# Kernel tuning notes

Measured on AMD Instinct MI355X. Metric: run time of the kernel, lower is better.

## Reference

```python
import jax, jax.numpy as jnp
import numpy as np
import math

WS = 7          # window_size
TOPK = 4        # routed regions
NUM_HEADS = 8   # only used for the scale factor (heads never split in forward)


def _dwconv(v_img, kernel, bias):
    # v_img: (N, ws, ws, C); kernel: (3, 3, 1, C) depthwise (groups=C), padding=1
    out = jax.lax.conv_general_dilated(
        v_img, kernel, window_strides=(1, 1), padding='SAME',
        dimension_numbers=('NHWC', 'HWIO', 'NHWC'),
        feature_group_count=v_img.shape[-1])
    return out + bias


def setup_inputs() -> dict:
    key = jax.random.key(0)
    ks = jax.random.split(key, 12)
    B, H, W, C = 8, 56, 56, 256
    std = 0.02
    return {
        'x': jax.random.normal(ks[0], (B, H, W, C), jnp.float32),
        'w_qkv': jax.random.normal(ks[1], (C, 3 * C), jnp.float32) * std,
        'b_qkv': jnp.zeros((3 * C,), jnp.float32),
        'w_g1': jax.random.normal(ks[2], (C, C // 4), jnp.float32) * std,
        'b_g1': jnp.zeros((C // 4,), jnp.float32),
        'w_g2': jax.random.normal(ks[3], (C // 4, 2), jnp.float32) * std,
        'b_g2': jnp.zeros((2,), jnp.float32),
        'dw_kernel': jax.random.normal(ks[4], (3, 3, 1, C), jnp.float32) * std,
        'dw_bias': jnp.zeros((C,), jnp.float32),
        'w_proj': jax.random.normal(ks[5], (C, C), jnp.float32) * std,
        'b_proj': jnp.zeros((C,), jnp.float32),
    }


def reference(x, w_qkv, b_qkv, w_g1, b_g1, w_g2, b_g2, dw_kernel, dw_bias, w_proj, b_proj):
    B, H, W, C = x.shape
    ws = WS
    nH, nW = H // ws, W // ws      # input chosen divisible by ws (pad path is no-op)
    S, ntok = nH * nW, ws * ws
    t = min(TOPK, S)
    scale = (C // NUM_HEADS) ** (-0.5)

    # window partition: (B, S, ws*ws, C)
    xw = x.reshape(B, nH, ws, nW, ws, C).transpose(0, 1, 3, 2, 4, 5).reshape(B, S, ntok, C)
    x_region = xw.mean(axis=2)                                  # (B, S, C)

    # region-level qkv and routing scores
    qkv_r = (x_region @ w_qkv + b_qkv).reshape(B, S, 3, C)
    q_r, k_r = qkv_r[:, :, 0], qkv_r[:, :, 1]
    A_r = jnp.einsum('bsc,bzc->bsz', q_r, k_r) * scale          # (B, S, S)
    _, topk_idx = jax.lax.top_k(A_r, t)                         # (B, S, t)

    # per-region Gaussian (diagonal covariance) weights over regions
    gp = jax.nn.relu(q_r @ w_g1 + b_g1) @ w_g2 + b_g2           # (B, S, 2)
    sigma = jax.nn.softplus(gp) + 0.5
    s_side = int(round(math.sqrt(S)))
    coords = jnp.arange(s_side, dtype=x.dtype)
    gy, gx = jnp.meshgrid(coords, coords, indexing='ij')
    mu = jnp.stack([gx.ravel(), gy.ravel()], axis=-1)           # (S, 2) as (x, y)
    d = mu[None, :, :] - mu[:, None, :]                         # (S, S, 2): mu_j - mu_i
    z = (d[..., 0][None] / sigma[..., 0][:, :, None]) ** 2 \
        + (d[..., 1][None] / sigma[..., 1][:, :, None]) ** 2    # (B, S, S)
    gauss = jnp.exp(-0.5 * z)
    gauss = gauss / (gauss.sum(-1, keepdims=True) + 1e-6)
    gwt = jnp.take_along_axis(gauss, topk_idx, axis=2)          # (B, S, t)

    # token-level qkv within windows
    qkv = (xw @ w_qkv + b_qkv).reshape(B, S, ntok, 3, C)
    q, k, v = qkv[..., 0, :], qkv[..., 1, :], qkv[..., 2, :]    # (B, S, ntok, C)

    # gather routed windows and reweight by Gaussian
    gather = jax.vmap(lambda a, i: a[i])                        # over batch
    k_g = (gather(k, topk_idx) * gwt[..., None, None]).reshape(B, S, t * ntok, C)
    v_g = (gather(v, topk_idx) * gwt[..., None, None]).reshape(B, S, t * ntok, C)

    attn = jax.nn.softmax(jnp.einsum('bswc,bskc->bswk', q, k_g) * scale, axis=-1)
    out = jnp.einsum('bswk,bskc->bswc', attn, v_g)              # (B, S, ntok, C)

    # depthwise-conv branch on v
    vdw = _dwconv(v.reshape(B * S, ws, ws, C), dw_kernel, dw_bias).reshape(B, S, ntok, C)
    out = out + vdw

    # window merge + output projection
    out = out.reshape(B, nH, nW, ws, ws, C).transpose(0, 1, 3, 2, 4, 5).reshape(B, H, W, C)
    return out @ w_proj + b_proj
```

## Files before the change

kernel.cpp:

```cpp
#include <hip/hip_runtime.h>
#include <math.h>

#define SCALE 0.17677669529663687f

typedef short short8 __attribute__((ext_vector_type(8)));
typedef float f32x4 __attribute__((ext_vector_type(4)));

__device__ __forceinline__ int token_row_addr(int m) {
    int b = m / 3136;
    int rem = m - b * 3136;
    int s = rem / 49;
    int tok = rem - s * 49;
    int h = (s >> 3) * 7 + tok / 7;
    int w = (s & 7) * 7 + (tok % 7);
    return (b * 56 + h) * 56 + w;
}

__device__ __forceinline__ void split2(float x, unsigned short& h, unsigned short& l) {
    unsigned int u = __float_as_uint(x);
    h = (unsigned short)(u >> 16);
    float hf = __uint_as_float(u & 0xFFFF0000u);
    l = (unsigned short)(__float_as_uint(x - hf) >> 16);
}

__device__ __forceinline__ unsigned int pack2(float x) {
    unsigned short h, l;
    split2(x, h, l);
    return ((unsigned int)h << 16) | l;
}

__device__ __forceinline__ float b2f(unsigned short u) {
    return __uint_as_float(((unsigned int)u) << 16);
}

__device__ __forceinline__ float unpack_f(unsigned int u) {
    return b2f((unsigned short)(u >> 16)) + b2f((unsigned short)(u & 0xFFFFu));
}

__device__ __forceinline__ void unpack_u4(uint4 a, uint4 b, short8& h, short8& l) {
    h[0] = (short)(a.x >> 16); l[0] = (short)(a.x & 0xFFFFu);
    h[1] = (short)(a.y >> 16); l[1] = (short)(a.y & 0xFFFFu);
    h[2] = (short)(a.z >> 16); l[2] = (short)(a.z & 0xFFFFu);
    h[3] = (short)(a.w >> 16); l[3] = (short)(a.w & 0xFFFFu);
    h[4] = (short)(b.x >> 16); l[4] = (short)(b.x & 0xFFFFu);
    h[5] = (short)(b.y >> 16); l[5] = (short)(b.y & 0xFFFFu);
    h[6] = (short)(b.z >> 16); l[6] = (short)(b.z & 0xFFFFu);
    h[7] = (short)(b.w >> 16); l[7] = (short)(b.w & 0xFFFFu);
}

__device__ __forceinline__ void load_unpack8(const unsigned int* g, short8& h, short8& l) {
    uint4 a = *(const uint4*)g;
    uint4 b = *(const uint4*)(g + 4);
    unpack_u4(a, b, h, l);
}

__device__ __forceinline__ void gload16(const unsigned short* g, unsigned short* l) {
    __builtin_amdgcn_global_load_lds(
        (const __attribute__((address_space(1))) unsigned int*)g,
        (__attribute__((address_space(3))) unsigned int*)l, 16, 0, 0);
}

__global__ void k_cvt_x(const float* __restrict__ x, unsigned short* __restrict__ xhi,
                        unsigned short* __restrict__ xlo) {
    int m = blockIdx.x;
    int k = threadIdx.x;
    float v = x[(size_t)token_row_addr(m) * 256 + k];
    unsigned short h, l;
    split2(v, h, l);
    xhi[(size_t)m * 256 + k] = h;
    xlo[(size_t)m * 256 + k] = l;
}

__global__ void k_cvt_w(const float* __restrict__ w, int ncols,
                        unsigned short* __restrict__ whi, unsigned short* __restrict__ wlo) {
    int n = blockIdx.x;
    int k = threadIdx.x;
    float v = w[(size_t)k * ncols + n];
    unsigned short h, l;
    split2(v, h, l);
    whi[(size_t)n * 256 + k] = h;
    wlo[(size_t)n * 256 + k] = l;
}

__global__ void k_region_mean(const float* __restrict__ x, float* __restrict__ xr) {
    int blk = blockIdx.x;
    int b = blk >> 6, s = blk & 63;
    int c = threadIdx.x;
    int hy0 = (s >> 3) * 7, wx0 = (s & 7) * 7;
    const float* xb = x + ((size_t)b * 56 * 56) * 256 + c;
    float sum = 0.f;
#pragma unroll 1
    for (int t = 0; t < 49; ++t) {
        int h = hy0 + t / 7, w = wx0 + (t % 7);
        sum += xb[(size_t)(h * 56 + w) * 256];
    }
    xr[(size_t)blk * 256 + c] = sum * (1.0f / 49.0f);
}

__global__ void k_region_qkv(const float* __restrict__ xr, const float* __restrict__ wqkv,
                             const float* __restrict__ bqkv, float* __restrict__ qkvr) {
    __shared__ float xs[256];
    int blk = blockIdx.x;
    int t = threadIdx.x;
    xs[t] = xr[(size_t)blk * 256 + t];
    __syncthreads();
    float a0 = 0.f, a1 = 0.f, a2 = 0.f;
#pragma unroll 4
    for (int k = 0; k < 256; ++k) {
        float xv = xs[k];
        const float* wrow = wqkv + (size_t)k * 768;
        a0 += xv * wrow[t];
        a1 += xv * wrow[t + 256];
        a2 += xv * wrow[t + 512];
    }
    float* o = qkvr + (size_t)blk * 768;
    o[t]       = a0 + bqkv[t];
    o[t + 256] = a1 + bqkv[t + 256];
    o[t + 512] = a2 + bqkv[t + 512];
}

__global__ void k_gating(const float* __restrict__ qkvr, const float* __restrict__ wg1,
                         const float* __restrict__ bg1, const float* __restrict__ wg2,
                         const float* __restrict__ bg2, float* __restrict__ sig) {
    __shared__ float hs[64];
    int blk = blockIdx.x;
    int j = threadIdx.x;
    const float* qr = qkvr + (size_t)blk * 768;
    float acc = bg1[j];
#pragma unroll 4
    for (int k = 0; k < 256; ++k) acc += qr[k] * wg1[(size_t)k * 64 + j];
    hs[j] = fmaxf(acc, 0.f);
    __syncthreads();
    if (j < 2) {
        float gp = bg2[j];
#pragma unroll 1
        for (int m = 0; m < 64; ++m) gp += hs[m] * wg2[m * 2 + j];
        float sp = fmaxf(gp, 0.f) + log1pf(expf(-fabsf(gp)));
        sig[blk * 2 + j] = sp + 0.5f;
    }
}

__global__ void k_topk_gauss(const float* __restrict__ qkvr, const float* __restrict__ sig,
                             int* __restrict__ topk, float* __restrict__ gwt) {
    __shared__ float A[64];
    __shared__ float G[64];
    __shared__ int idxs[4];
    __shared__ float gsum_s;
    int blk = blockIdx.x;
    int b = blk >> 6, s = blk & 63;
    int z = threadIdx.x;
    const float* qr = qkvr + (size_t)blk * 768;
    const float* kr = qkvr + (size_t)(b * 64 + z) * 768 + 256;
    float acc = 0.f;
#pragma unroll 4
    for (int k = 0; k < 256; k += 4) {
        float4 q4 = *(const float4*)(qr + k);
        float4 k4 = *(const float4*)(kr + k);
        acc += q4.x * k4.x + q4.y * k4.y + q4.z * k4.z + q4.w * k4.w;
    }
    A[z] = acc * SCALE;
    float s0 = sig[blk * 2 + 0], s1 = sig[blk * 2 + 1];
    float dx = (float)((z & 7) - (s & 7));
    float dy = (float)((z >> 3) - (s >> 3));
    float t0 = dx / s0, t1 = dy / s1;
    float zz = t0 * t0 + t1 * t1;
    G[z] = expf(-0.5f * zz);
    __syncthreads();
    if (z == 0) {
        float gs = 0.f;
        for (int m = 0; m < 64; ++m) gs += G[m];
        gsum_s = gs + 1e-6f;
        for (int it = 0; it < 4; ++it) {
            int best = 0;
            float bv = A[0];
            for (int m = 1; m < 64; ++m) {
                if (A[m] > bv) { bv = A[m]; best = m; }
            }
            idxs[it] = best;
            A[best] = -3.0e38f;
        }
    }
    __syncthreads();
    if (z < 4) {
        int id = idxs[z];
        topk[blk * 4 + z] = id;
        gwt[blk * 4 + z] = G[id] / gsum_s;
    }
}

__global__ __launch_bounds__(256) void k_mm_qkv(
    const unsigned short* __restrict__ xhi, const unsigned short* __restrict__ xlo,
    const unsigned short* __restrict__ whi, const unsigned short* __restrict__ wlo,
    const float* __restrict__ bqkv,
    unsigned int* __restrict__ Qp, unsigned int* __restrict__ Kp,
    unsigned int* __restrict__ Vp) {
    __shared__ __align__(16) unsigned short Ah[4096];
    __shared__ __align__(16) unsigned short Al[4096];
    __shared__ __align__(16) unsigned short Bh[4096];
    __shared__ __align__(16) unsigned short Bl[4096];
    int tid = threadIdx.x;
    int ln = tid & 63, wv = tid >> 6;
    int m0 = blockIdx.y * 128, n0 = blockIdx.x * 128;
    int mrow = (wv >> 1) * 64, ncol = (wv & 1) * 64;

    int lrow = ln >> 2, lseg = (ln & 3) * 8;
    const unsigned short* gA0 = xhi + (size_t)(m0 + wv * 32 + lrow) * 256 + lseg;
    const unsigned short* gA1 = gA0 + 16 * 256;
    const unsigned short* gAl0 = xlo + (size_t)(m0 + wv * 32 + lrow) * 256 + lseg;
    const unsigned short* gAl1 = gAl0 + 16 * 256;
    const unsigned short* gB0 = whi + (size_t)(n0 + wv * 32 + lrow) * 256 + lseg;
    const unsigned short* gB1 = gB0 + 16 * 256;
    const unsigned short* gBl0 = wlo + (size_t)(n0 + wv * 32 + lrow) * 256 + lseg;
    const unsigned short* gBl1 = gBl0 + 16 * 256;
    unsigned short* lA0 = &Ah[(wv * 32) * 32];
    unsigned short* lA1 = &Ah[(wv * 32 + 16) * 32];
    unsigned short* lAl0 = &Al[(wv * 32) * 32];
    unsigned short* lAl1 = &Al[(wv * 32 + 16) * 32];
    unsigned short* lB0 = &Bh[(wv * 32) * 32];
    unsigned short* lB1 = &Bh[(wv * 32 + 16) * 32];
    unsigned short* lBl0 = &Bl[(wv * 32) * 32];
    unsigned short* lBl1 = &Bl[(wv * 32 + 16) * 32];

    int fm = ln & 15, fq = (ln >> 4) * 8;
    f32x4 acc[4][4];
#pragma unroll
    for (int i = 0; i < 4; ++i)
#pragma unroll
        for (int j = 0; j < 4; ++j) acc[i][j] = (f32x4){0.f, 0.f, 0.f, 0.f};

#pragma unroll 1
    for (int kc = 0; kc < 8; ++kc) {
        if (kc) __syncthreads();
        gload16(gA0, lA0); gload16(gA1, lA1);
        gload16(gAl0, lAl0); gload16(gAl1, lAl1);
        gload16(gB0, lB0); gload16(gB1, lB1);
        gload16(gBl0, lBl0); gload16(gBl1, lBl1);
        gA0 += 32; gA1 += 32; gAl0 += 32; gAl1 += 32;
        gB0 += 32; gB1 += 32; gBl0 += 32; gBl1 += 32;
        __syncthreads();

        short8 ah[4], bh[4], xx[4];
#pragma unroll
        for (int mi = 0; mi < 4; ++mi)
            ah[mi] = *(const short8*)&Ah[(mrow + mi * 16 + fm) * 32 + fq];
#pragma unroll
        for (int ni = 0; ni < 4; ++ni)
            bh[ni] = *(const short8*)&Bh[(ncol + ni * 16 + fm) * 32 + fq];
#pragma unroll
        for (int mi = 0; mi < 4; ++mi)
#pragma unroll
            for (int ni = 0; ni < 4; ++ni)
                acc[mi][ni] = __builtin_amdgcn_mfma_f32_16x16x32_bf16(ah[mi], bh[ni], acc[mi][ni], 0, 0, 0);
#pragma unroll
        for (int mi = 0; mi < 4; ++mi)
            xx[mi] = *(const short8*)&Al[(mrow + mi * 16 + fm) * 32 + fq];
#pragma unroll
        for (int mi = 0; mi < 4; ++mi)
#pragma unroll
            for (int ni = 0; ni < 4; ++ni)
                acc[mi][ni] = __builtin_amdgcn_mfma_f32_16x16x32_bf16(xx[mi], bh[ni], acc[mi][ni], 0, 0, 0);
#pragma unroll
        for (int ni = 0; ni < 4; ++ni)
            xx[ni] = *(const short8*)&Bl[(ncol + ni * 16 + fm) * 32 + fq];
#pragma unroll
        for (int mi = 0; mi < 4; ++mi)
#pragma unroll
            for (int ni = 0; ni < 4; ++ni)
                acc[mi][ni] = __builtin_amdgcn_mfma_f32_16x16x32_bf16(ah[mi], xx[ni], acc[mi][ni], 0, 0, 0);
    }

    int nb = n0 >> 7;
    unsigned int* dst = (nb < 2) ? Qp : (nb < 4) ? Kp : Vp;
    int qrow = (ln >> 4) * 4;
#pragma unroll
    for (int ni = 0; ni < 4; ++ni) {
        int col = (n0 & 255) + ncol + ni * 16 + fm;
        float bias = bqkv[n0 + ncol + ni * 16 + fm];
#pragma unroll
        for (int mi = 0; mi < 4; ++mi) {
#pragma unroll
            for (int r = 0; r < 4; ++r) {
                int m = m0 + mrow + mi * 16 + qrow + r;
                dst[(size_t)m * 256 + col] = pack2(acc[mi][ni][r] + bias);
            }
        }
    }
}

__global__ __launch_bounds__(256) void k_transpose_v(
    const unsigned int* __restrict__ Vp, unsigned int* __restrict__ Vtp) {
    __shared__ unsigned int T[49][257];
    int win = blockIdx.x;
    int tid = threadIdx.x;
#pragma unroll 1
    for (int i = tid; i < 49 * 64; i += 256) {
        int tok = i >> 6, cq = (i & 63) * 4;
        uint4 v = *(const uint4*)&Vp[((size_t)win * 49 + tok) * 256 + cq];
        T[tok][cq + 0] = v.x;
        T[tok][cq + 1] = v.y;
        T[tok][cq + 2] = v.z;
        T[tok][cq + 3] = v.w;
    }
    __syncthreads();
#pragma unroll 1
    for (int it = 0; it < 8; ++it) {
        int item = tid + it * 256;
        int c = item >> 3, t8 = (item & 7) * 8;
        uint4 o0, o1;
        o0.x = (t8 + 0 < 49) ? T[t8 + 0][c] : 0u;
        o0.y = (t8 + 1 < 49) ? T[t8 + 1][c] : 0u;
        o0.z = (t8 + 2 < 49) ? T[t8 + 2][c] : 0u;
        o0.w = (t8 + 3 < 49) ? T[t8 + 3][c] : 0u;
        o1.x = (t8 + 4 < 49) ? T[t8 + 4][c] : 0u;
        o1.y = (t8 + 5 < 49) ? T[t8 + 5][c] : 0u;
        o1.z = (t8 + 6 < 49) ? T[t8 + 6][c] : 0u;
        o1.w = (t8 + 7 < 49) ? T[t8 + 7][c] : 0u;
        size_t o = (size_t)win * 16384 + (size_t)c * 64 + t8;
        *(uint4*)&Vtp[o] = o0;
        *(uint4*)&Vtp[o + 4] = o1;
    }
}

__global__ __launch_bounds__(256) void k_attn_logits2(
    const unsigned int* __restrict__ Qp, const unsigned int* __restrict__ Kp,
    const int* __restrict__ topk, const float* __restrict__ gwt,
    unsigned int* __restrict__ Pp) {
    __shared__ float redm[4][64];
    __shared__ float reds[4][64];
    __shared__ float gmax[64];
    __shared__ float ginv[64];
    int blk = blockIdx.x;
    int win = ((blk & 7) << 6) | (blk >> 3);
    int b = win >> 6;
    int tid = threadIdx.x, ln = tid & 63, wv = tid >> 6;
    int fm = ln & 15, g = ln >> 4, fq = g * 8;

    int myreg = topk[win * 4 + wv];
    float gw = gwt[win * 4 + wv];
    float sg = SCALE * gw;
    size_t qbase = (size_t)win * 49 * 256;
    size_t kbase = (size_t)(b * 64 + myreg) * 49 * 256;

    f32x4 acc[4][4];
#pragma unroll
    for (int i = 0; i < 4; ++i)
#pragma unroll
        for (int j = 0; j < 4; ++j) acc[i][j] = (f32x4){0.f, 0.f, 0.f, 0.f};

#pragma unroll 1
    for (int kc = 0; kc < 256; kc += 32) {
        short8 ah[4], al[4], bh[4], bl[4];
#pragma unroll
        for (int mi = 0; mi < 4; ++mi)
            load_unpack8(&Qp[qbase + (size_t)(mi * 16 + fm) * 256 + kc + fq], ah[mi], al[mi]);
#pragma unroll
        for (int ni = 0; ni < 4; ++ni)
            load_unpack8(&Kp[kbase + (size_t)(ni * 16 + fm) * 256 + kc + fq], bh[ni], bl[ni]);
#pragma unroll
        for (int mi = 0; mi < 4; ++mi)
#pragma unroll
            for (int ni = 0; ni < 4; ++ni) {
                acc[mi][ni] = __builtin_amdgcn_mfma_f32_16x16x32_bf16(ah[mi], bh[ni], acc[mi][ni], 0, 0, 0);
                acc[mi][ni] = __builtin_amdgcn_mfma_f32_16x16x32_bf16(al[mi], bh[ni], acc[mi][ni], 0, 0, 0);
                acc[mi][ni] = __builtin_amdgcn_mfma_f32_16x16x32_bf16(ah[mi], bl[ni], acc[mi][ni], 0, 0, 0);
            }
    }

#pragma unroll
    for (int mi = 0; mi < 4; ++mi)
#pragma unroll
        for (int ni = 0; ni < 4; ++ni) acc[mi][ni] *= sg;

    float rmax[4][4];
#pragma unroll
    for (int mi = 0; mi < 4; ++mi)
#pragma unroll
        for (int r = 0; r < 4; ++r) rmax[mi][r] = -3.0e38f;
#pragma unroll
    for (int mi = 0; mi < 4; ++mi)
#pragma unroll
        for (int ni = 0; ni < 4; ++ni) {
            if (ni * 16 + fm < 49) {
#pragma unroll
                for (int r = 0; r < 4; ++r)
                    rmax[mi][r] = fmaxf(rmax[mi][r], acc[mi][ni][r]);
            }
        }
#pragma unroll
    for (int off = 1; off < 16; off <<= 1)
#pragma unroll
        for (int mi = 0; mi < 4; ++mi)
#pragma unroll
            for (int r = 0; r < 4; ++r)
                rmax[mi][r] = fmaxf(rmax[mi][r], __shfl_xor(rmax[mi][r], off, 64));
    if (fm == 0) {
#pragma unroll
        for (int mi = 0; mi < 4; ++mi)
#pragma unroll
            for (int r = 0; r < 4; ++r)
                redm[wv][mi * 16 + g * 4 + r] = rmax[mi][r];
    }
    __syncthreads();
    if (tid < 64)
        gmax[tid] = fmaxf(fmaxf(redm[0][tid], redm[1][tid]),
                          fmaxf(redm[2][tid], redm[3][tid]));
    __syncthreads();

    float gm[4][4];
#pragma unroll
    for (int mi = 0; mi < 4; ++mi)
#pragma unroll
        for (int r = 0; r < 4; ++r) gm[mi][r] = gmax[mi * 16 + g * 4 + r];
    float rsum[4][4];
#pragma unroll
    for (int mi = 0; mi < 4; ++mi)
#pragma unroll
        for (int r = 0; r < 4; ++r) rsum[mi][r] = 0.f;
#pragma unroll
    for (int mi = 0; mi < 4; ++mi)
#pragma unroll
        for (int ni = 0; ni < 4; ++ni) {
            bool valid = (ni * 16 + fm) < 49;
#pragma unroll
            for (int r = 0; r < 4; ++r) {
                float e = valid ? __expf(acc[mi][ni][r] - gm[mi][r]) : 0.f;
                acc[mi][ni][r] = e;
                rsum[mi][r] += e;
            }
        }
#pragma unroll
    for (int off = 1; off < 16; off <<= 1)
#pragma unroll
        for (int mi = 0; mi < 4; ++mi)
#pragma unroll
            for (int r = 0; r < 4; ++r)
                rsum[mi][r] += __shfl_xor(rsum[mi][r], off, 64);
    if (fm == 0) {
#pragma unroll
        for (int mi = 0; mi < 4; ++mi)
#pragma unroll
            for (int r = 0; r < 4; ++r)
                reds[wv][mi * 16 + g * 4 + r] = rsum[mi][r];
    }
    __syncthreads();
    if (tid < 64)
        ginv[tid] = 1.0f / (reds[0][tid] + reds[1][tid] + reds[2][tid] + reds[3][tid]);
    __syncthreads();

    size_t pbase = (size_t)win * 16384 + wv * 64;
#pragma unroll
    for (int mi = 0; mi < 4; ++mi) {
#pragma unroll
        for (int r = 0; r < 4; ++r) {
            int row = mi * 16 + g * 4 + r;
            float giv = (row < 49) ? ginv[row] * gw : 0.f;
#pragma unroll
            for (int ni = 0; ni < 4; ++ni) {
                float p = acc[mi][ni][r] * giv;
                Pp[pbase + (size_t)row * 256 + ni * 16 + fm] = pack2(p);
            }
        }
    }
}

__global__ __launch_bounds__(256) void k_attn_pv2(
    const unsigned int* __restrict__ Pp, const unsigned int* __restrict__ Vtp,
    const unsigned int* __restrict__ Vp,
    const int* __restrict__ topk, const float* __restrict__ dwk,
    const float* __restrict__ dwb, unsigned int* __restrict__ ATTp) {
    __shared__ unsigned int Vs[49][258];
    int blk = blockIdx.x;
    int win = ((blk & 7) << 6) | (blk >> 3);
    int b = win >> 6;
    int tid = threadIdx.x, ln = tid & 63, wv = tid >> 6;
    int fm = ln & 15, g = ln >> 4, fq = g * 8;
    int ncol = wv * 64;
    size_t pbase = (size_t)win * 16384;

#pragma unroll 1
    for (int i = tid; i < 49 * 64; i += 256) {
        int tok = i >> 6, cq = (i & 63) * 4;
        uint4 v = *(const uint4*)&Vp[((size_t)win * 49 + tok) * 256 + cq];
        Vs[tok][cq + 0] = v.x;
        Vs[tok][cq + 1] = v.y;
        Vs[tok][cq + 2] = v.z;
        Vs[tok][cq + 3] = v.w;
    }
    __syncthreads();

    f32x4 oacc[4][4];
#pragma unroll
    for (int i = 0; i < 4; ++i)
#pragma unroll
        for (int j = 0; j < 4; ++j) oacc[i][j] = (f32x4){0.f, 0.f, 0.f, 0.f};

#pragma unroll 1
    for (int r = 0; r < 4; ++r) {
        int reg = topk[win * 4 + r];
        size_t vbase = (size_t)(b * 64 + reg) * 16384;
#pragma unroll
        for (int half = 0; half < 2; ++half) {
            int kc = r * 64 + half * 32;
            int tokoff = half * 32;
            short8 ah[4], al[4], bh[4], bl[4];
#pragma unroll
            for (int mi = 0; mi < 4; ++mi)
                load_unpack8(&Pp[pbase + (size_t)(mi * 16 + fm) * 256 + kc + fq], ah[mi], al[mi]);
#pragma unroll
            for (int ni = 0; ni < 4; ++ni)
                load_unpack8(&Vtp[vbase + (size_t)(ncol + ni * 16 + fm) * 64 + tokoff + fq], bh[ni], bl[ni]);
#pragma unroll
            for (int mi = 0; mi < 4; ++mi)
#pragma unroll
                for (int ni = 0; ni < 4; ++ni) {
                    oacc[mi][ni] = __builtin_amdgcn_mfma_f32_16x16x32_bf16(ah[mi], bh[ni], oacc[mi][ni], 0, 0, 0);
                    oacc[mi][ni] = __builtin_amdgcn_mfma_f32_16x16x32_bf16(al[mi], bh[ni], oacc[mi][ni], 0, 0, 0);
                    oacc[mi][ni] = __builtin_amdgcn_mfma_f32_16x16x32_bf16(ah[mi], bl[ni], oacc[mi][ni], 0, 0, 0);
                }
        }
    }

#pragma unroll 1
    for (int ni = 0; ni < 4; ++ni) {
        int c = ncol + ni * 16 + fm;
        float dk[9];
#pragma unroll
        for (int t = 0; t < 9; ++t) dk[t] = dwk[(size_t)t * 256 + c];
        float db = dwb[c];
#pragma unroll
        for (int mi = 0; mi < 4; ++mi) {
#pragma unroll
            for (int rr = 0; rr < 4; ++rr) {
                int w = mi * 16 + g * 4 + rr;
                if (w < 49) {
                    int py = w / 7, px = w - py * 7;
                    float vd = db;
#pragma unroll
                    for (int dy = 0; dy < 3; ++dy) {
                        int yy = py + dy - 1;
                        if (yy < 0 || yy > 6) continue;
#pragma unroll
                        for (int dx = 0; dx < 3; ++dx) {
                            int xx = px + dx - 1;
                            if (xx < 0 || xx > 6) continue;
                            vd += unpack_f(Vs[yy * 7 + xx][c]) * dk[dy * 3 + dx];
                        }
                    }
                    ATTp[((size_t)win * 49 + w) * 256 + c] = pack2(oacc[mi][ni][rr] + vd);
                }
            }
        }
    }
}

__global__ __launch_bounds__(256) void k_mm_proj(
    const unsigned int* __restrict__ Ap,
    const unsigned short* __restrict__ whi, const unsigned short* __restrict__ wlo,
    const float* __restrict__ bp, float* __restrict__ out) {
    __shared__ __align__(16) unsigned int As[128 * 36];
    __shared__ __align__(16) unsigned short Bh[4096];
    __shared__ __align__(16) unsigned short Bl[4096];
    int tid = threadIdx.x;
    int ln = tid & 63, wv = tid >> 6;
    int m0 = blockIdx.y * 128, n0 = blockIdx.x * 128;
    int mrow = (wv >> 1) * 64, ncol = (wv & 1) * 64;

    int lrow = ln >> 2, lseg = (ln & 3) * 8;
    const unsigned short* gB0 = whi + (size_t)(n0 + wv * 32 + lrow) * 256 + lseg;
    const unsigned short* gB1 = gB0 + 16 * 256;
    const unsigned short* gBl0 = wlo + (size_t)(n0 + wv * 32 + lrow) * 256 + lseg;
    const unsigned short* gBl1 = gBl0 + 16 * 256;
    unsigned short* lB0 = &Bh[(wv * 32) * 32];
    unsigned short* lB1 = &Bh[(wv * 32 + 16) * 32];
    unsigned short* lBl0 = &Bl[(wv * 32) * 32];
    unsigned short* lBl1 = &Bl[(wv * 32 + 16) * 32];

    int arow = ln >> 3, akk = (ln & 7) * 4;
    int fm = ln & 15, fq = (ln >> 4) * 8;
    f32x4 acc[4][4];
#pragma unroll
    for (int i = 0; i < 4; ++i)
#pragma unroll
        for (int j = 0; j < 4; ++j) acc[i][j] = (f32x4){0.f, 0.f, 0.f, 0.f};

#pragma unroll 1
    for (int kc = 0; kc < 8; ++kc) {
        if (kc) __syncthreads();
        gload16(gB0, lB0); gload16(gB1, lB1);
        gload16(gBl0, lBl0); gload16(gBl1, lBl1);
        gB0 += 32; gB1 += 32; gBl0 += 32; gBl1 += 32;
#pragma unroll
        for (int it = 0; it < 4; ++it) {
            int row = wv * 32 + it * 8 + arow;
            uint4 v = *(const uint4*)&Ap[(size_t)(m0 + row) * 256 + kc * 32 + akk];
            *(uint4*)&As[row * 36 + akk] = v;
        }
        __syncthreads();

        short8 ah[4], al[4], bh[4], xx[4];
#pragma unroll
        for (int mi = 0; mi < 4; ++mi) {
            const unsigned int* p = &As[(mrow + mi * 16 + fm) * 36 + fq];
            unpack_u4(*(const uint4*)p, *(const uint4*)(p + 4), ah[mi], al[mi]);
        }
#pragma unroll
        for (int ni = 0; ni < 4; ++ni)
            bh[ni] = *(const short8*)&Bh[(ncol + ni * 16 + fm) * 32 + fq];
#pragma unroll
        for (int mi = 0; mi < 4; ++mi)
#pragma unroll
            for (int ni = 0; ni < 4; ++ni)
                acc[mi][ni] = __builtin_amdgcn_mfma_f32_16x16x32_bf16(ah[mi], bh[ni], acc[mi][ni], 0, 0, 0);
#pragma unroll
        for (int mi = 0; mi < 4; ++mi)
#pragma unroll
            for (int ni = 0; ni < 4; ++ni)
                acc[mi][ni] = __builtin_amdgcn_mfma_f32_16x16x32_bf16(al[mi], bh[ni], acc[mi][ni], 0, 0, 0);
#pragma unroll
        for (int ni = 0; ni < 4; ++ni)
            xx[ni] = *(const short8*)&Bl[(ncol + ni * 16 + fm) * 32 + fq];
#pragma unroll
        for (int mi = 0; mi < 4; ++mi)
#pragma unroll
            for (int ni = 0; ni < 4; ++ni)
                acc[mi][ni] = __builtin_amdgcn_mfma_f32_16x16x32_bf16(ah[mi], xx[ni], acc[mi][ni], 0, 0, 0);
    }

    int qrow = (ln >> 4) * 4;
#pragma unroll
    for (int mi = 0; mi < 4; ++mi) {
#pragma unroll
        for (int r = 0; r < 4; ++r) {
            int m = m0 + mrow + mi * 16 + qrow + r;
            size_t orow = (size_t)token_row_addr(m);
#pragma unroll
            for (int ni = 0; ni < 4; ++ni) {
                int col = n0 + ncol + ni * 16 + fm;
                out[orow * 256 + col] = acc[mi][ni][r] + bp[col];
            }
        }
    }
}

extern "C" void kernel_launch(void* const* d_in, const int* in_sizes, int n_in,
                              void* d_out, int out_size, void* d_ws, size_t ws_size,
                              hipStream_t stream) {
    const float* x    = (const float*)d_in[0];
    const float* wqkv = (const float*)d_in[1];
    const float* bqkv = (const float*)d_in[2];
    const float* wg1  = (const float*)d_in[3];
    const float* bg1  = (const float*)d_in[4];
    const float* wg2  = (const float*)d_in[5];
    const float* bg2  = (const float*)d_in[6];
    const float* dwk  = (const float*)d_in[7];
    const float* dwb  = (const float*)d_in[8];
    const float* wp   = (const float*)d_in[9];
    const float* bp   = (const float*)d_in[10];
    float* out = (float*)d_out;

    const size_t NTOT = (size_t)25088 * 256;
    const size_t VTSZ = (size_t)512 * 256 * 64;
    unsigned int* Qp  = (unsigned int*)d_ws;
    unsigned int* Kp  = Qp + NTOT;
    unsigned int* Vp  = Kp + NTOT;
    unsigned int* Vtp = Vp + NTOT;
    unsigned int* Pp  = Vtp + VTSZ;
    unsigned short* XH = (unsigned short*)(Pp + VTSZ);
    unsigned short* XL = XH + NTOT;
    unsigned int* ATTp = (unsigned int*)XH;
    unsigned short* WQH = XL + NTOT;
    unsigned short* WQL = WQH + 768 * 256;
    unsigned short* WPH = WQL + 768 * 256;
    unsigned short* WPL = WPH + 256 * 256;
    float* XR   = (float*)(WPL + 256 * 256);
    float* QKVR = XR + 512 * 256;
    float* SIG  = QKVR + 512 * 768;
    float* GWT  = SIG + 1024;
    int*   TOPK = (int*)(GWT + 2048);

    hipLaunchKernelGGL(k_cvt_x, dim3(25088), dim3(256), 0, stream, x, XH, XL);
    hipLaunchKernelGGL(k_cvt_w, dim3(768), dim3(256), 0, stream, wqkv, 768, WQH, WQL);
    hipLaunchKernelGGL(k_cvt_w, dim3(256), dim3(256), 0, stream, wp, 256, WPH, WPL);
    hipLaunchKernelGGL(k_region_mean, dim3(512), dim3(256), 0, stream, x, XR);
    hipLaunchKernelGGL(k_region_qkv, dim3(512), dim3(256), 0, stream, XR, wqkv, bqkv, QKVR);
    hipLaunchKernelGGL(k_gating, dim3(512), dim3(64), 0, stream, QKVR, wg1, bg1, wg2, bg2, SIG);
    hipLaunchKernelGGL(k_topk_gauss, dim3(512), dim3(64), 0, stream, QKVR, SIG, TOPK, GWT);
    hipLaunchKernelGGL(k_mm_qkv, dim3(6, 196), dim3(256), 0, stream,
                       XH, XL, WQH, WQL, bqkv, Qp, Kp, Vp);
    hipLaunchKernelGGL(k_transpose_v, dim3(512), dim3(256), 0, stream, Vp, Vtp);
    hipLaunchKernelGGL(k_attn_logits2, dim3(512), dim3(256), 0, stream,
                       Qp, Kp, TOPK, GWT, Pp);
    hipLaunchKernelGGL(k_attn_pv2, dim3(512), dim3(256), 0, stream,
                       Pp, Vtp, Vp, TOPK, dwk, dwb, ATTp);
    hipLaunchKernelGGL(k_mm_proj, dim3(2, 196), dim3(256), 0, stream,
                       ATTp, WPH, WPL, bp, out);
}
```

Before: 374.9 us.

## Split attention kernels into row halves and fuse region mean, qkv and gating

```diff
diff --git a/kernel.cpp b/kernel.cpp
--- a/kernel.cpp
+++ b/kernel.cpp
@@ -82,28 +82,28 @@
     wlo[(size_t)n * 256 + k] = l;
 }
 
-__global__ void k_region_mean(const float* __restrict__ x, float* __restrict__ xr) {
+__global__ void k_region_fused(const float* __restrict__ x, const float* __restrict__ wqkv,
+                               const float* __restrict__ bqkv, const float* __restrict__ wg1,
+                               const float* __restrict__ bg1, const float* __restrict__ wg2,
+                               const float* __restrict__ bg2, float* __restrict__ qkvr,
+                               float* __restrict__ sig) {
+    __shared__ float xs[256];
+    __shared__ float qbuf[256];
+    __shared__ float hs[64];
     int blk = blockIdx.x;
     int b = blk >> 6, s = blk & 63;
-    int c = threadIdx.x;
+    int t = threadIdx.x;
     int hy0 = (s >> 3) * 7, wx0 = (s & 7) * 7;
-    const float* xb = x + ((size_t)b * 56 * 56) * 256 + c;
+    const float* xb = x + ((size_t)b * 56 * 56) * 256 + t;
     float sum = 0.f;
 #pragma unroll 1
-    for (int t = 0; t < 49; ++t) {
-        int h = hy0 + t / 7, w = wx0 + (t % 7);
+    for (int tt = 0; tt < 49; ++tt) {
+        int h = hy0 + tt / 7, w = wx0 + (tt % 7);
         sum += xb[(size_t)(h * 56 + w) * 256];
     }
-    xr[(size_t)blk * 256 + c] = sum * (1.0f / 49.0f);
-}
-
-__global__ void k_region_qkv(const float* __restrict__ xr, const float* __restrict__ wqkv,
-                             const float* __restrict__ bqkv, float* __restrict__ qkvr) {
-    __shared__ float xs[256];
-    int blk = blockIdx.x;
-    int t = threadIdx.x;
-    xs[t] = xr[(size_t)blk * 256 + t];
-    __syncthreads();
+    xs[t] = sum * (1.0f / 49.0f);
+    __syncthreads();
+
     float a0 = 0.f, a1 = 0.f, a2 = 0.f;
 #pragma unroll 4
     for (int k = 0; k < 256; ++k) {
@@ -113,30 +113,27 @@
         a1 += xv * wrow[t + 256];
         a2 += xv * wrow[t + 512];
     }
+    float q = a0 + bqkv[t];
+    qbuf[t] = q;
     float* o = qkvr + (size_t)blk * 768;
-    o[t]       = a0 + bqkv[t];
+    o[t]       = q;
     o[t + 256] = a1 + bqkv[t + 256];
     o[t + 512] = a2 + bqkv[t + 512];
-}
-
-__global__ void k_gating(const float* __restrict__ qkvr, const float* __restrict__ wg1,
-                         const float* __restrict__ bg1, const float* __restrict__ wg2,
-                         const float* __restrict__ bg2, float* __restrict__ sig) {
-    __shared__ float hs[64];
-    int blk = blockIdx.x;
-    int j = threadIdx.x;
-    const float* qr = qkvr + (size_t)blk * 768;
-    float acc = bg1[j];
+    __syncthreads();
+
+    if (t < 64) {
+        float acc = bg1[t];
 #pragma unroll 4
-    for (int k = 0; k < 256; ++k) acc += qr[k] * wg1[(size_t)k * 64 + j];
-    hs[j] = fmaxf(acc, 0.f);
-    __syncthreads();
-    if (j < 2) {
-        float gp = bg2[j];
-#pragma unroll 1
-        for (int m = 0; m < 64; ++m) gp += hs[m] * wg2[m * 2 + j];
+        for (int k = 0; k < 256; ++k) acc += qbuf[k] * wg1[(size_t)k * 64 + t];
+        hs[t] = fmaxf(acc, 0.f);
+    }
+    __syncthreads();
+    if (t < 2) {
+        float gp = bg2[t];
+#pragma unroll 1
+        for (int m = 0; m < 64; ++m) gp += hs[m] * wg2[m * 2 + t];
         float sp = fmaxf(gp, 0.f) + log1pf(expf(-fabsf(gp)));
-        sig[blk * 2 + j] = sp + 0.5f;
+        sig[blk * 2 + t] = sp + 0.5f;
     }
 }
 
@@ -325,13 +322,15 @@
     const unsigned int* __restrict__ Qp, const unsigned int* __restrict__ Kp,
     const int* __restrict__ topk, const float* __restrict__ gwt,
     unsigned int* __restrict__ Pp) {
-    __shared__ float redm[4][64];
-    __shared__ float reds[4][64];
-    __shared__ float gmax[64];
-    __shared__ float ginv[64];
+    __shared__ float redm[4][32];
+    __shared__ float reds[4][32];
+    __shared__ float gmax[32];
+    __shared__ float ginv[32];
     int blk = blockIdx.x;
-    int win = ((blk & 7) << 6) | (blk >> 3);
-    int b = win >> 6;
+    int batch = blk & 7, idx = blk >> 3;
+    int win = (batch << 6) | (idx >> 1);
+    int wh = idx & 1;
+    int b = batch;
     int tid = threadIdx.x, ln = tid & 63, wv = tid >> 6;
     int fm = ln & 15, g = ln >> 4, fq = g * 8;
 
@@ -341,23 +340,33 @@
     size_t qbase = (size_t)win * 49 * 256;
     size_t kbase = (size_t)(b * 64 + myreg) * 49 * 256;
 
-    f32x4 acc[4][4];
-#pragma unroll
-    for (int i = 0; i < 4; ++i)
+    int arow[2];
+#pragma unroll
+    for (int mi = 0; mi < 2; ++mi) {
+        int w = wh * 32 + mi * 16 + fm;
+        arow[mi] = (w < 49) ? w : 48;
+    }
+
+    f32x4 acc[2][4];
+#pragma unroll
+    for (int i = 0; i < 2; ++i)
 #pragma unroll
         for (int j = 0; j < 4; ++j) acc[i][j] = (f32x4){0.f, 0.f, 0.f, 0.f};
 
 #pragma unroll 1
     for (int kc = 0; kc < 256; kc += 32) {
-        short8 ah[4], al[4], bh[4], bl[4];
-#pragma unroll
-        for (int mi = 0; mi < 4; ++mi)
-            load_unpack8(&Qp[qbase + (size_t)(mi * 16 + fm) * 256 + kc + fq], ah[mi], al[mi]);
-#pragma unroll
-        for (int ni = 0; ni < 4; ++ni)
-            load_unpack8(&Kp[kbase + (size_t)(ni * 16 + fm) * 256 + kc + fq], bh[ni], bl[ni]);
-#pragma unroll
-        for (int mi = 0; mi < 4; ++mi)
+        short8 ah[2], al[2], bh[4], bl[4];
+#pragma unroll
+        for (int mi = 0; mi < 2; ++mi)
+            load_unpack8(&Qp[qbase + (size_t)arow[mi] * 256 + kc + fq], ah[mi], al[mi]);
+#pragma unroll
+        for (int ni = 0; ni < 4; ++ni) {
+            int tok = ni * 16 + fm;
+            int trow = (tok < 49) ? tok : 48;
+            load_unpack8(&Kp[kbase + (size_t)trow * 256 + kc + fq], bh[ni], bl[ni]);
+        }
+#pragma unroll
+        for (int mi = 0; mi < 2; ++mi)
 #pragma unroll
             for (int ni = 0; ni < 4; ++ni) {
                 acc[mi][ni] = __builtin_amdgcn_mfma_f32_16x16x32_bf16(ah[mi], bh[ni], acc[mi][ni], 0, 0, 0);
@@ -367,17 +376,17 @@
     }
 
 #pragma unroll
-    for (int mi = 0; mi < 4; ++mi)
+    for (int mi = 0; mi < 2; ++mi)
 #pragma unroll
         for (int ni = 0; ni < 4; ++ni) acc[mi][ni] *= sg;
 
-    float rmax[4][4];
-#pragma unroll
-    for (int mi = 0; mi < 4; ++mi)
+    float rmax[2][4];
+#pragma unroll
+    for (int mi = 0; mi < 2; ++mi)
 #pragma unroll
         for (int r = 0; r < 4; ++r) rmax[mi][r] = -3.0e38f;
 #pragma unroll
-    for (int mi = 0; mi < 4; ++mi)
+    for (int mi = 0; mi < 2; ++mi)
 #pragma unroll
         for (int ni = 0; ni < 4; ++ni) {
             if (ni * 16 + fm < 49) {
@@ -389,35 +398,35 @@
 #pragma unroll
     for (int off = 1; off < 16; off <<= 1)
 #pragma unroll
-        for (int mi = 0; mi < 4; ++mi)
+        for (int mi = 0; mi < 2; ++mi)
 #pragma unroll
             for (int r = 0; r < 4; ++r)
                 rmax[mi][r] = fmaxf(rmax[mi][r], __shfl_xor(rmax[mi][r], off, 64));
     if (fm == 0) {
 #pragma unroll
-        for (int mi = 0; mi < 4; ++mi)
+        for (int mi = 0; mi < 2; ++mi)
 #pragma unroll
             for (int r = 0; r < 4; ++r)
                 redm[wv][mi * 16 + g * 4 + r] = rmax[mi][r];
     }
     __syncthreads();
-    if (tid < 64)
+    if (tid < 32)
         gmax[tid] = fmaxf(fmaxf(redm[0][tid], redm[1][tid]),
                           fmaxf(redm[2][tid], redm[3][tid]));
     __syncthreads();
 
-    float gm[4][4];
-#pragma unroll
-    for (int mi = 0; mi < 4; ++mi)
+    float gm[2][4];
+#pragma unroll
+    for (int mi = 0; mi < 2; ++mi)
 #pragma unroll
         for (int r = 0; r < 4; ++r) gm[mi][r] = gmax[mi * 16 + g * 4 + r];
-    float rsum[4][4];
-#pragma unroll
-    for (int mi = 0; mi < 4; ++mi)
+    float rsum[2][4];
+#pragma unroll
+    for (int mi = 0; mi < 2; ++mi)
 #pragma unroll
         for (int r = 0; r < 4; ++r) rsum[mi][r] = 0.f;
 #pragma unroll
-    for (int mi = 0; mi < 4; ++mi)
+    for (int mi = 0; mi < 2; ++mi)
 #pragma unroll
         for (int ni = 0; ni < 4; ++ni) {
             bool valid = (ni * 16 + fm) < 49;
@@ -431,33 +440,34 @@
 #pragma unroll
     for (int off = 1; off < 16; off <<= 1)
 #pragma unroll
-        for (int mi = 0; mi < 4; ++mi)
+        for (int mi = 0; mi < 2; ++mi)
 #pragma unroll
             for (int r = 0; r < 4; ++r)
                 rsum[mi][r] += __shfl_xor(rsum[mi][r], off, 64);
     if (fm == 0) {
 #pragma unroll
-        for (int mi = 0; mi < 4; ++mi)
+        for (int mi = 0; mi < 2; ++mi)
 #pragma unroll
             for (int r = 0; r < 4; ++r)
                 reds[wv][mi * 16 + g * 4 + r] = rsum[mi][r];
     }
     __syncthreads();
-    if (tid < 64)
+    if (tid < 32)
         ginv[tid] = 1.0f / (reds[0][tid] + reds[1][tid] + reds[2][tid] + reds[3][tid]);
     __syncthreads();
 
     size_t pbase = (size_t)win * 16384 + wv * 64;
 #pragma unroll
-    for (int mi = 0; mi < 4; ++mi) {
+    for (int mi = 0; mi < 2; ++mi) {
 #pragma unroll
         for (int r = 0; r < 4; ++r) {
-            int row = mi * 16 + g * 4 + r;
-            float giv = (row < 49) ? ginv[row] * gw : 0.f;
+            int rowb = mi * 16 + g * 4 + r;
+            int w = wh * 32 + rowb;
+            float giv = (w < 49) ? ginv[rowb] * gw : 0.f;
 #pragma unroll
             for (int ni = 0; ni < 4; ++ni) {
                 float p = acc[mi][ni][r] * giv;
-                Pp[pbase + (size_t)row * 256 + ni * 16 + fm] = pack2(p);
+                Pp[pbase + (size_t)w * 256 + ni * 16 + fm] = pack2(p);
             }
         }
     }
@@ -468,29 +478,33 @@
     const unsigned int* __restrict__ Vp,
     const int* __restrict__ topk, const float* __restrict__ dwk,
     const float* __restrict__ dwb, unsigned int* __restrict__ ATTp) {
-    __shared__ unsigned int Vs[49][258];
+    __shared__ unsigned int Vs[42][258];
     int blk = blockIdx.x;
-    int win = ((blk & 7) << 6) | (blk >> 3);
-    int b = win >> 6;
+    int batch = blk & 7, idx = blk >> 3;
+    int win = (batch << 6) | (idx >> 1);
+    int wh = idx & 1;
+    int b = batch;
     int tid = threadIdx.x, ln = tid & 63, wv = tid >> 6;
     int fm = ln & 15, g = ln >> 4, fq = g * 8;
     int ncol = wv * 64;
     size_t pbase = (size_t)win * 16384;
 
-#pragma unroll 1
-    for (int i = tid; i < 49 * 64; i += 256) {
-        int tok = i >> 6, cq = (i & 63) * 4;
+    int lo = wh ? 21 : 0;
+    int cnt = wh ? 28 : 42;
+#pragma unroll 1
+    for (int i = tid; i < cnt * 64; i += 256) {
+        int tok = lo + (i >> 6), cq = (i & 63) * 4;
         uint4 v = *(const uint4*)&Vp[((size_t)win * 49 + tok) * 256 + cq];
-        Vs[tok][cq + 0] = v.x;
-        Vs[tok][cq + 1] = v.y;
-        Vs[tok][cq + 2] = v.z;
-        Vs[tok][cq + 3] = v.w;
-    }
-    __syncthreads();
-
-    f32x4 oacc[4][4];
-#pragma unroll
-    for (int i = 0; i < 4; ++i)
+        Vs[tok - lo][cq + 0] = v.x;
+        Vs[tok - lo][cq + 1] = v.y;
+        Vs[tok - lo][cq + 2] = v.z;
+        Vs[tok - lo][cq + 3] = v.w;
+    }
+    __syncthreads();
+
+    f32x4 oacc[2][4];
+#pragma unroll
+    for (int i = 0; i < 2; ++i)
 #pragma unroll
         for (int j = 0; j < 4; ++j) oacc[i][j] = (f32x4){0.f, 0.f, 0.f, 0.f};
 
@@ -502,15 +516,15 @@
         for (int half = 0; half < 2; ++half) {
             int kc = r * 64 + half * 32;
             int tokoff = half * 32;
-            short8 ah[4], al[4], bh[4], bl[4];
-#pragma unroll
-            for (int mi = 0; mi < 4; ++mi)
-                load_unpack8(&Pp[pbase + (size_t)(mi * 16 + fm) * 256 + kc + fq], ah[mi], al[mi]);
+            short8 ah[2], al[2], bh[4], bl[4];
+#pragma unroll
+            for (int mi = 0; mi < 2; ++mi)
+                load_unpack8(&Pp[pbase + (size_t)(wh * 32 + mi * 16 + fm) * 256 + kc + fq], ah[mi], al[mi]);
 #pragma unroll
             for (int ni = 0; ni < 4; ++ni)
                 load_unpack8(&Vtp[vbase + (size_t)(ncol + ni * 16 + fm) * 64 + tokoff + fq], bh[ni], bl[ni]);
 #pragma unroll
-            for (int mi = 0; mi < 4; ++mi)
+            for (int mi = 0; mi < 2; ++mi)
 #pragma unroll
                 for (int ni = 0; ni < 4; ++ni) {
                     oacc[mi][ni] = __builtin_amdgcn_mfma_f32_16x16x32_bf16(ah[mi], bh[ni], oacc[mi][ni], 0, 0, 0);
@@ -528,10 +542,10 @@
         for (int t = 0; t < 9; ++t) dk[t] = dwk[(size_t)t * 256 + c];
         float db = dwb[c];
 #pragma unroll
-        for (int mi = 0; mi < 4; ++mi) {
+        for (int mi = 0; mi < 2; ++mi) {
 #pragma unroll
             for (int rr = 0; rr < 4; ++rr) {
-                int w = mi * 16 + g * 4 + rr;
+                int w = wh * 32 + mi * 16 + g * 4 + rr;
                 if (w < 49) {
                     int py = w / 7, px = w - py * 7;
                     float vd = db;
@@ -543,7 +557,7 @@
                         for (int dx = 0; dx < 3; ++dx) {
                             int xx = px + dx - 1;
                             if (xx < 0 || xx > 6) continue;
-                            vd += unpack_f(Vs[yy * 7 + xx][c]) * dk[dy * 3 + dx];
+                            vd += unpack_f(Vs[yy * 7 + xx - lo][c]) * dk[dy * 3 + dx];
                         }
                     }
                     ATTp[((size_t)win * 49 + w) * 256 + c] = pack2(oacc[mi][ni][rr] + vd);
@@ -672,8 +686,7 @@
     unsigned short* WQL = WQH + 768 * 256;
     unsigned short* WPH = WQL + 768 * 256;
     unsigned short* WPL = WPH + 256 * 256;
-    float* XR   = (float*)(WPL + 256 * 256);
-    float* QKVR = XR + 512 * 256;
+    float* QKVR = (float*)(WPL + 256 * 256);
     float* SIG  = QKVR + 512 * 768;
     float* GWT  = SIG + 1024;
     int*   TOPK = (int*)(GWT + 2048);
@@ -681,16 +694,15 @@
     hipLaunchKernelGGL(k_cvt_x, dim3(25088), dim3(256), 0, stream, x, XH, XL);
     hipLaunchKernelGGL(k_cvt_w, dim3(768), dim3(256), 0, stream, wqkv, 768, WQH, WQL);
     hipLaunchKernelGGL(k_cvt_w, dim3(256), dim3(256), 0, stream, wp, 256, WPH, WPL);
-    hipLaunchKernelGGL(k_region_mean, dim3(512), dim3(256), 0, stream, x, XR);
-    hipLaunchKernelGGL(k_region_qkv, dim3(512), dim3(256), 0, stream, XR, wqkv, bqkv, QKVR);
-    hipLaunchKernelGGL(k_gating, dim3(512), dim3(64), 0, stream, QKVR, wg1, bg1, wg2, bg2, SIG);
+    hipLaunchKernelGGL(k_region_fused, dim3(512), dim3(256), 0, stream,
+                       x, wqkv, bqkv, wg1, bg1, wg2, bg2, QKVR, SIG);
     hipLaunchKernelGGL(k_topk_gauss, dim3(512), dim3(64), 0, stream, QKVR, SIG, TOPK, GWT);
     hipLaunchKernelGGL(k_mm_qkv, dim3(6, 196), dim3(256), 0, stream,
                        XH, XL, WQH, WQL, bqkv, Qp, Kp, Vp);
     hipLaunchKernelGGL(k_transpose_v, dim3(512), dim3(256), 0, stream, Vp, Vtp);
-    hipLaunchKernelGGL(k_attn_logits2, dim3(512), dim3(256), 0, stream,
+    hipLaunchKernelGGL(k_attn_logits2, dim3(1024), dim3(256), 0, stream,
                        Qp, Kp, TOPK, GWT, Pp);
-    hipLaunchKernelGGL(k_attn_pv2, dim3(512), dim3(256), 0, stream,
+    hipLaunchKernelGGL(k_attn_pv2, dim3(1024), dim3(256), 0, stream,
                        Pp, Vtp, Vp, TOPK, dwk, dwb, ATTp);
     hipLaunchKernelGGL(k_mm_proj, dim3(2, 196), dim3(256), 0, stream,
                        ATTp, WPH, WPL, bp, out);
```

New measurement: 366.0 us. 1.02x faster.
